# Kernel tuning notes

Measured on AMD Instinct MI355X. Metric: run time of the kernel, lower is better.

The kernel has to match this reference:

```python
import jax, jax.numpy as jnp
import numpy as np

N, H, W = 1, 60, 60


def _collect_idx(H, W):
    oh = np.arange(H)[:, None, None, None]
    ow = np.arange(W)[None, :, None, None]
    h = np.arange(H)[None, None, :, None]
    w = np.arange(W)[None, None, None, :]
    idx = (oh + H - 1 - h) * (2 * W - 1) + (ow + W - 1 - w)
    return jnp.asarray(idx.reshape(H * W, H, W), dtype=jnp.int32)


def setup_inputs() -> dict:
    key = jax.random.key(0)
    c_in = (2 * H - 1) * (2 * W - 1)
    x = jax.random.normal(key, (N, c_in, H, W), dtype=jnp.float32)
    return {"x": x}


def reference(x):
    n, cm, h, w = x.shape
    idx = _collect_idx(h, w)[None]
    idx = jnp.broadcast_to(idx, (n, h * w, h, w))
    return jnp.take_along_axis(x, idx, axis=1)
```

## Files before the change

### kernel.cpp

```cpp
#include <hip/hip_runtime.h>


#define CH_STRIDE 3600

__global__ __launch_bounds__(256) void psa_collect_kernel(
    const float* __restrict__ x, float* __restrict__ out) {

    __shared__ float lds[119 * 60];

    const int blk = blockIdx.x;
    const int oh  = blk / 60;
    const int h   = blk - oh * 60;
    const int a   = oh - h + 59;
    const int tid = threadIdx.x;

    const float* src = x + (size_t)a * 119 * CH_STRIDE + h * 60;
    for (int l = tid; l < 119 * 15; l += 256) {
        const int b  = l / 15;
        const int j4 = (l - b * 15) * 4;
        const int w0 = (b < 59) ? (59 - b) : 0;
        const int w1 = (b < 59) ? 60 : (119 - b);
        if (j4 < w1 && j4 + 4 > w0) {
            const float4 v =
                *reinterpret_cast<const float4*>(src + (size_t)b * CH_STRIDE + j4);
            *reinterpret_cast<float4*>(&lds[b * 60 + j4]) = v;
        }
    }
    __syncthreads();

    float* dst = out + (size_t)(oh * 60) * CH_STRIDE + h * 60;
    for (int m = tid; m < 900; m += 256) {
        const int ow   = m / 15;
        const int w    = (m - ow * 15) * 4;
        const int base = (ow + 59) * 60;
        float4 v;
        v.x = lds[base - 59 * w];
        v.y = lds[base - 59 * (w + 1)];
        v.z = lds[base - 59 * (w + 2)];
        v.w = lds[base - 59 * (w + 3)];
        *reinterpret_cast<float4*>(dst + (size_t)ow * CH_STRIDE + w) = v;
    }
}

extern "C" void kernel_launch(void* const* d_in, const int* in_sizes, int n_in,
                              void* d_out, int out_size, void* d_ws, size_t ws_size,
                              hipStream_t stream) {
    const float* x = (const float*)d_in[0];
    float* out = (float*)d_out;
    psa_collect_kernel<<<dim3(3600), dim3(256), 0, stream>>>(x, out);
}
```

Before: 32.30 us.

## Process two rows per block, transpose on LDS write, and swizzle block order

Each block now handles two consecutive h rows, so its output writes cover 480 contiguous bytes per output channel instead of 240. The diagonal transpose moves from the LDS read side to the LDS write side, which lets the output stage use plain float4 LDS reads and float4 global stores. Block indices are swizzled so that blocks likely to run on the same XCD get contiguous work. The cost is twice the LDS per block, which lowers occupancy, and scalar scattered LDS stores during the load stage.

```diff
diff --git a/kernel.cpp b/kernel.cpp
--- a/kernel.cpp
+++ b/kernel.cpp
@@ -6,39 +6,47 @@
 __global__ __launch_bounds__(256) void psa_collect_kernel(
     const float* __restrict__ x, float* __restrict__ out) {
 
-    __shared__ float lds[119 * 60];
+    __shared__ float lds[2][3600];
 
-    const int blk = blockIdx.x;
-    const int oh  = blk / 60;
-    const int h   = blk - oh * 60;
-    const int a   = oh - h + 59;
+    int l = blockIdx.x;
+    l = (l & 7) * 225 + (l >> 3);
+    const int oh = l / 30;
+    const int hp = l - oh * 30;
+    const int h0 = hp * 2;
     const int tid = threadIdx.x;
 
-    const float* src = x + (size_t)a * 119 * CH_STRIDE + h * 60;
-    for (int l = tid; l < 119 * 15; l += 256) {
-        const int b  = l / 15;
-        const int j4 = (l - b * 15) * 4;
-        const int w0 = (b < 59) ? (59 - b) : 0;
-        const int w1 = (b < 59) ? 60 : (119 - b);
-        if (j4 < w1 && j4 + 4 > w0) {
-            const float4 v =
-                *reinterpret_cast<const float4*>(src + (size_t)b * CH_STRIDE + j4);
-            *reinterpret_cast<float4*>(&lds[b * 60 + j4]) = v;
+    for (int hh = 0; hh < 2; ++hh) {
+        const int h = h0 + hh;
+        const int a = oh + 59 - h;
+        const float* src = x + (size_t)a * 119 * CH_STRIDE + h * 60;
+        for (int t = tid; t < 119 * 15; t += 256) {
+            const int b  = t / 15;
+            const int j4 = (t - b * 15) * 4;
+            const int w0 = (b < 59) ? (59 - b) : 0;
+            const int w1 = (b < 59) ? 60 : (119 - b);
+            if (j4 < w1 && j4 + 4 > w0) {
+                const float4 v =
+                    *reinterpret_cast<const float4*>(src + (size_t)b * CH_STRIDE + j4);
+                const float* ve = reinterpret_cast<const float*>(&v);
+#pragma unroll
+                for (int e = 0; e < 4; ++e) {
+                    const int w = j4 + e;
+                    const int d = b + w - 59;
+                    if ((unsigned)d < 60u) lds[hh][d * 60 + w] = ve[e];
+                }
+            }
         }
     }
     __syncthreads();
 
-    float* dst = out + (size_t)(oh * 60) * CH_STRIDE + h * 60;
-    for (int m = tid; m < 900; m += 256) {
-        const int ow   = m / 15;
-        const int w    = (m - ow * 15) * 4;
-        const int base = (ow + 59) * 60;
-        float4 v;
-        v.x = lds[base - 59 * w];
-        v.y = lds[base - 59 * (w + 1)];
-        v.z = lds[base - 59 * (w + 2)];
-        v.w = lds[base - 59 * (w + 3)];
-        *reinterpret_cast<float4*>(dst + (size_t)ow * CH_STRIDE + w) = v;
+    float* dst = out + (size_t)(oh * 60) * CH_STRIDE + h0 * 60;
+    for (int m = tid; m < 1800; m += 256) {
+        const int ow = m / 30;
+        const int r  = m - ow * 30;
+        const int hh = r / 15;
+        const int j4 = (r - hh * 15) * 4;
+        const float4 v = *reinterpret_cast<const float4*>(&lds[hh][ow * 60 + j4]);
+        *reinterpret_cast<float4*>(dst + (size_t)ow * CH_STRIDE + hh * 60 + j4) = v;
     }
 }
 
@@ -47,5 +55,5 @@
                               hipStream_t stream) {
     const float* x = (const float*)d_in[0];
     float* out = (float*)d_out;
-    psa_collect_kernel<<<dim3(3600), dim3(256), 0, stream>>>(x, out);
+    psa_collect_kernel<<<dim3(1800), dim3(256), 0, stream>>>(x, out);
 }
```

New measurement: 30.97 us. 1.04x faster.
